# Kernel optimization log

Hardware: AMD Instinct MI355X
Metric: run time of the kernel (lower is better)

The kernel has to match this reference:

```python
import jax, jax.numpy as jnp
import numpy as np

N_NODES = 50000
N_EDGES = 400000
IN_DIM = 8
HIDDEN = 768
N_LAYERS = 4
LN_EPS = 1e-5


def setup_inputs() -> dict:
    key = jax.random.key(0)
    ks = jax.random.split(key, 10)
    x = jax.random.normal(ks[0], (N_NODES, IN_DIM), dtype=jnp.float32)
    edge_index = jax.random.randint(ks[1], (2, N_EDGES), 0, N_NODES, dtype=jnp.int32)
    # input projection
    s_in = 1.0 / np.sqrt(IN_DIM)
    Wp = jax.random.uniform(ks[2], (HIDDEN, IN_DIM), jnp.float32, -s_in, s_in)
    bp = jax.random.uniform(ks[3], (HIDDEN,), jnp.float32, -s_in, s_in)
    # stacked per-layer SAGEConv params (all layers have out_c == HIDDEN here)
    s_h = 1.0 / np.sqrt(HIDDEN)
    Wl = jax.random.uniform(ks[4], (N_LAYERS, HIDDEN, HIDDEN), jnp.float32, -s_h, s_h)  # lin_l (aggregated neighbors), has bias
    bl = jax.random.uniform(ks[5], (N_LAYERS, HIDDEN), jnp.float32, -s_h, s_h)
    Wr = jax.random.uniform(ks[6], (N_LAYERS, HIDDEN, HIDDEN), jnp.float32, -s_h, s_h)  # lin_r (root), no bias
    # LayerNorm params
    gamma = jnp.ones((N_LAYERS, HIDDEN), dtype=jnp.float32)
    beta = jnp.zeros((N_LAYERS, HIDDEN), dtype=jnp.float32)
    return {"x": x, "Wp": Wp, "bp": bp, "Wl": Wl, "bl": bl, "Wr": Wr,
            "gamma": gamma, "beta": beta, "edge_index": edge_index}


def _layer_norm(h, g, b):
    mu = jnp.mean(h, axis=-1, keepdims=True)
    var = jnp.mean(jnp.square(h - mu), axis=-1, keepdims=True)
    return (h - mu) * jax.lax.rsqrt(var + LN_EPS) * g + b


def reference(x, Wp, bp, Wl, bl, Wr, gamma, beta, edge_index):
    n = x.shape[0]
    src, dst = edge_index[0], edge_index[1]
    # in-degree per target node, clamped for mean
    deg = jax.ops.segment_sum(jnp.ones_like(dst, dtype=x.dtype), dst, num_segments=n)
    inv_deg = 1.0 / jnp.maximum(deg, 1.0)

    h = x @ Wp.T + bp  # [N, HIDDEN]

    def layer(h, params):
        Wl_i, bl_i, Wr_i, g_i, b_i = params
        # mean aggregation of source features at targets: [N, C]
        agg = jax.ops.segment_sum(h[src], dst, num_segments=n) * inv_deg[:, None]
        out = agg @ Wl_i.T + bl_i + h @ Wr_i.T  # SAGEConv
        out = _layer_norm(jax.nn.silu(out), g_i, b_i)  # norm(silu(conv))
        return out, None

    h, _ = jax.lax.scan(layer, h, (Wl, bl, Wr, gamma, beta))
    return h
```

## Files before the change

kernel.cpp:

```cpp
#include <hip/hip_runtime.h>

#define NN 50000
#define NE 400000
#define HID 768
#define NL 4

typedef short bf16x8_t __attribute__((ext_vector_type(8)));
typedef float f32x4_t __attribute__((ext_vector_type(4)));

__device__ __forceinline__ unsigned short f2bf(float f) {
  union { float f; unsigned int u; } c; c.f = f;
  unsigned int u = c.u;
  u += 0x7FFF + ((u >> 16) & 1);
  return (unsigned short)(u >> 16);
}
__device__ __forceinline__ float bf2f(unsigned short s) {
  union { unsigned int u; float f; } c; c.u = ((unsigned int)s) << 16;
  return c.f;
}

__device__ __forceinline__ void async16(const void* g, void* l) {
  __builtin_amdgcn_global_load_lds((const __attribute__((address_space(1))) void*)g,
                                   (__attribute__((address_space(3))) void*)l,
                                   16, 0, 0);
}

__global__ void k_zero2(int* __restrict__ a, int* __restrict__ b, int n) {
  int i = blockIdx.x * blockDim.x + threadIdx.x;
  if (i < n) { a[i] = 0; b[i] = 0; }
}

__global__ void k_cvt(const float* __restrict__ a, unsigned short* __restrict__ o, int n) {
  int i = blockIdx.x * blockDim.x + threadIdx.x;
  if (i < n) o[i] = f2bf(a[i]);
}

__global__ __launch_bounds__(256) void k_inproj(const float* __restrict__ x,
                                                const float* __restrict__ Wp,
                                                const float* __restrict__ bp,
                                                unsigned short* __restrict__ h) {
  int n = blockIdx.x;
  __shared__ float xs[8];
  if (threadIdx.x < 8) xs[threadIdx.x] = x[n * 8 + threadIdx.x];
  __syncthreads();
  for (int j = threadIdx.x; j < HID; j += 256) {
    const float* w = Wp + j * 8;
    float s = bp[j];
#pragma unroll
    for (int k = 0; k < 8; ++k) s += xs[k] * w[k];
    h[(size_t)n * HID + j] = f2bf(s);
  }
}

__global__ void k_deg(const int* __restrict__ dst, int* __restrict__ deg) {
  int i = blockIdx.x * blockDim.x + threadIdx.x;
  if (i < NE) atomicAdd(&deg[dst[i]], 1);
}

__global__ __launch_bounds__(1024) void k_scan(const int* __restrict__ deg, int* __restrict__ rowptr) {
  __shared__ int sm[1024];
  const int chunk = 49;
  int t = threadIdx.x;
  int start = t * chunk;
  int end = min(start + chunk, NN);
  int local = 0;
  for (int i = start; i < end; ++i) local += deg[i];
  sm[t] = local;
  __syncthreads();
  for (int off = 1; off < 1024; off <<= 1) {
    int v = (t >= off) ? sm[t - off] : 0;
    __syncthreads();
    sm[t] += v;
    __syncthreads();
  }
  int run = sm[t] - local;
  for (int i = start; i < end; ++i) { rowptr[i] = run; run += deg[i]; }
  if (start < NN && end == NN) rowptr[NN] = run;
}

__global__ void k_fill(const int* __restrict__ src, const int* __restrict__ dst,
                       const int* __restrict__ rowptr, int* __restrict__ cursor,
                       int* __restrict__ csr) {
  int i = blockIdx.x * blockDim.x + threadIdx.x;
  if (i < NE) {
    int d = dst[i];
    int pos = atomicAdd(&cursor[d], 1);
    csr[rowptr[d] + pos] = src[i];
  }
}

__global__ __launch_bounds__(192) void k_agg(const unsigned short* __restrict__ h,
                                             const int* __restrict__ csr,
                                             const int* __restrict__ rowptr,
                                             unsigned short* __restrict__ agg) {
  int n = blockIdx.x;
  int t = threadIdx.x;
  int beg = rowptr[n], end = rowptr[n + 1];
  float a0 = 0.f, a1 = 0.f, a2 = 0.f, a3 = 0.f;
  for (int i = beg; i < end; ++i) {
    int s = csr[i];
    ushort4 v = *(const ushort4*)(h + (size_t)s * HID + t * 4);
    a0 += bf2f(v.x); a1 += bf2f(v.y); a2 += bf2f(v.z); a3 += bf2f(v.w);
  }
  float inv = 1.0f / (float)max(end - beg, 1);
  ushort4 o;
  o.x = f2bf(a0 * inv); o.y = f2bf(a1 * inv); o.z = f2bf(a2 * inv); o.w = f2bf(a3 * inv);
  *(ushort4*)(agg + (size_t)n * HID + t * 4) = o;
}

#define BM 128
#define BN 128
#define BK 32
#define NBAND 391

__global__ __launch_bounds__(256) void k_gemm(const unsigned short* __restrict__ A0,
                                              const unsigned short* __restrict__ A1,
                                              const unsigned short* __restrict__ B0,
                                              const unsigned short* __restrict__ B1,
                                              const float* __restrict__ bias,
                                              unsigned short* __restrict__ sact, int M) {
  int b = blockIdx.x;
  int xcd = b & 7;
  int rest = b >> 3;
  int nt6 = rest % 6;
  int g = rest / 6;
  int mband = g * 8 + xcd;
  if (mband >= NBAND) return;
  int m0 = mband * BM;
  int n0 = nt6 * BN;

  __shared__ unsigned short As[BM * BK];
  __shared__ unsigned short Bs[BN * BK];
  f32x4_t acc[4][4] = {};
  int tid = threadIdx.x;
  int lane = tid & 63, w = tid >> 6;
  int wr = w >> 1, wc = w & 1;
  int r4 = lane >> 2;
  int cg = (lane & 3) ^ ((lane >> 3) & 3);
  int cs = cg * 8;

  for (int phase = 0; phase < 2; ++phase) {
    const unsigned short* A = phase ? A1 : A0;
    const unsigned short* B = phase ? B1 : B0;
    for (int k0 = 0; k0 < HID; k0 += BK) {
      __syncthreads();
#pragma unroll
      for (int c = 0; c < 2; ++c) {
        int seg = w * 32 + c * 16;
        int row = seg + r4;
        async16(A + (size_t)(m0 + row) * HID + k0 + cs, &As[seg * BK]);
        async16(B + (size_t)(n0 + row) * HID + k0 + cs, &Bs[seg * BK]);
      }
      __syncthreads();
      bf16x8_t af[4], bfr[4];
      int q = lane >> 4;
      int mr = lane & 15;
      int sq = (q ^ ((mr >> 1) & 3)) * 8;
#pragma unroll
      for (int t = 0; t < 4; ++t) {
        af[t]  = *(const bf16x8_t*)(&As[(wr * 64 + t * 16 + mr) * BK + sq]);
        bfr[t] = *(const bf16x8_t*)(&Bs[(wc * 64 + t * 16 + mr) * BK + sq]);
      }
#pragma unroll
      for (int mt = 0; mt < 4; ++mt)
#pragma unroll
        for (int nt = 0; nt < 4; ++nt)
          acc[mt][nt] = __builtin_amdgcn_mfma_f32_16x16x32_bf16(af[mt], bfr[nt], acc[mt][nt], 0, 0, 0);
    }
  }
  int col = lane & 15;
  int rq = (lane >> 4) * 4;
#pragma unroll
  for (int mt = 0; mt < 4; ++mt) {
#pragma unroll
    for (int nt = 0; nt < 4; ++nt) {
      int j = n0 + wc * 64 + nt * 16 + col;
      float bv = bias[j];
#pragma unroll
      for (int r = 0; r < 4; ++r) {
        int gm = m0 + wr * 64 + mt * 16 + rq + r;
        if (gm < M) {
          float v = acc[mt][nt][r] + bv;
          float s = v / (1.f + __expf(-v));
          sact[(size_t)gm * HID + j] = f2bf(s);
        }
      }
    }
  }
}

__global__ __launch_bounds__(256) void k_ln(const unsigned short* __restrict__ sact,
                                            const float* __restrict__ gamma,
                                            const float* __restrict__ beta,
                                            unsigned short* __restrict__ hout,
                                            float* __restrict__ fout) {
  int n = blockIdx.x;
  const unsigned short* p = sact + (size_t)n * HID;
  float v[3];
  float sum = 0.f, sq = 0.f;
#pragma unroll
  for (int i = 0; i < 3; ++i) {
    float s = bf2f(p[threadIdx.x + i * 256]);
    v[i] = s; sum += s; sq += s * s;
  }
#pragma unroll
  for (int off = 32; off >= 1; off >>= 1) {
    sum += __shfl_down(sum, off);
    sq  += __shfl_down(sq, off);
  }
  __shared__ float rs[4], rq2[4];
  int wv = threadIdx.x >> 6;
  if ((threadIdx.x & 63) == 0) { rs[wv] = sum; rq2[wv] = sq; }
  __syncthreads();
  if (threadIdx.x == 0) {
    float s = rs[0] + rs[1] + rs[2] + rs[3];
    float q = rq2[0] + rq2[1] + rq2[2] + rq2[3];
    rs[0] = s / (float)HID;
    rq2[0] = q / (float)HID;
  }
  __syncthreads();
  float mu = rs[0];
  float var = rq2[0] - mu * mu;
  float inv = rsqrtf(var + 1e-5f);
#pragma unroll
  for (int i = 0; i < 3; ++i) {
    int j = threadIdx.x + i * 256;
    float y = (v[i] - mu) * inv * gamma[j] + beta[j];
    if (fout) fout[(size_t)n * HID + j] = y;
    else      hout[(size_t)n * HID + j] = f2bf(y);
  }
}

extern "C" void kernel_launch(void* const* d_in, const int* in_sizes, int n_in,
                              void* d_out, int out_size, void* d_ws, size_t ws_size,
                              hipStream_t stream) {
  const float* x     = (const float*)d_in[0];
  const float* Wp    = (const float*)d_in[1];
  const float* bp    = (const float*)d_in[2];
  const float* Wl    = (const float*)d_in[3];
  const float* bl    = (const float*)d_in[4];
  const float* Wr    = (const float*)d_in[5];
  const float* gamma = (const float*)d_in[6];
  const float* beta  = (const float*)d_in[7];
  const int*   ei    = (const int*)d_in[8];
  float* out = (float*)d_out;

  const int* src = ei;
  const int* dst = ei + NE;

  char* p = (char*)d_ws;
  unsigned short* h    = (unsigned short*)p;              p += (size_t)NN * HID * 2;
  unsigned short* agg  = (unsigned short*)p;              p += (size_t)NN * HID * 2;
  unsigned short* sact = (unsigned short*)p;              p += (size_t)NN * HID * 2;
  unsigned short* Wlb  = (unsigned short*)p;              p += (size_t)NL * HID * HID * 2;
  unsigned short* Wrb  = (unsigned short*)p;              p += (size_t)NL * HID * HID * 2;
  int* deg             = (int*)p;                         p += (size_t)NN * 4;
  int* rowptr          = (int*)p;                         p += (size_t)(NN + 1) * 4 + 12;
  int* cursor          = (int*)p;                         p += (size_t)NN * 4;
  int* csr             = (int*)p;                         p += (size_t)NE * 4;

  k_zero2<<<(NN + 255) / 256, 256, 0, stream>>>(deg, cursor, NN);
  int wn = NL * HID * HID;
  k_cvt<<<(wn + 255) / 256, 256, 0, stream>>>(Wl, Wlb, wn);
  k_cvt<<<(wn + 255) / 256, 256, 0, stream>>>(Wr, Wrb, wn);
  k_inproj<<<NN, 256, 0, stream>>>(x, Wp, bp, h);
  k_deg<<<(NE + 255) / 256, 256, 0, stream>>>(dst, deg);
  k_scan<<<1, 1024, 0, stream>>>(deg, rowptr);
  k_fill<<<(NE + 255) / 256, 256, 0, stream>>>(src, dst, rowptr, cursor, csr);

  int ggrid = 8 * 6 * ((NBAND + 7) / 8);
  for (int l = 0; l < NL; ++l) {
    k_agg<<<NN, 192, 0, stream>>>(h, csr, rowptr, agg);
    k_gemm<<<ggrid, 256, 0, stream>>>(agg, h,
                                      Wlb + (size_t)l * HID * HID,
                                      Wrb + (size_t)l * HID * HID,
                                      bl + (size_t)l * HID, sact, NN);
    k_ln<<<NN, 256, 0, stream>>>(sact, gamma + (size_t)l * HID, beta + (size_t)l * HID,
                                 h, (l == NL - 1) ? out : nullptr);
  }
}
```

Measured before the change: 1.701 ms.

## Enlarge GEMM tiles to 224x256 and double-buffer async LDS loads

Replaces the 128x128 GEMM tile with a 224x256 tile computed by 512 threads. The two K phases (aggregated and root inputs) are fused into one 48-step loop. Global-to-LDS async loads are double-buffered, with explicit vmcnt waits and MFMA priority raised, so loads for step T+2 overlap compute on step T. The intent is more operand reuse per tile and better latency hiding, at the cost of higher register and LDS pressure. Each stage loads 256 A rows even though only 224 are used, so the last band reads past the end of the input rows.

```diff
diff --git a/kernel.cpp b/kernel.cpp
--- a/kernel.cpp
+++ b/kernel.cpp
@@ -108,77 +108,107 @@
   *(ushort4*)(agg + (size_t)n * HID + t * 4) = o;
 }
 
-#define BM 128
-#define BN 128
-#define BK 32
-#define NBAND 391
-
-__global__ __launch_bounds__(256) void k_gemm(const unsigned short* __restrict__ A0,
-                                              const unsigned short* __restrict__ A1,
-                                              const unsigned short* __restrict__ B0,
-                                              const unsigned short* __restrict__ B1,
-                                              const float* __restrict__ bias,
-                                              unsigned short* __restrict__ sact, int M) {
+#define BM 224
+#define BN 256
+#define BKT 32
+#define NKT 48
+#define NBANDS 224
+
+__global__ __launch_bounds__(512, 2) void k_gemm(const unsigned short* __restrict__ A0,
+                                                 const unsigned short* __restrict__ A1,
+                                                 const unsigned short* __restrict__ B0,
+                                                 const unsigned short* __restrict__ B1,
+                                                 const float* __restrict__ bias,
+                                                 unsigned short* __restrict__ sact, int M) {
+  __shared__ __align__(16) unsigned short As[2][256 * BKT];
+  __shared__ __align__(16) unsigned short Bs[2][256 * BKT];
+
   int b = blockIdx.x;
   int xcd = b & 7;
   int rest = b >> 3;
-  int nt6 = rest % 6;
-  int g = rest / 6;
+  int nt3 = rest % 3;
+  int g = rest / 3;
   int mband = g * 8 + xcd;
-  if (mband >= NBAND) return;
   int m0 = mband * BM;
-  int n0 = nt6 * BN;
-
-  __shared__ unsigned short As[BM * BK];
-  __shared__ unsigned short Bs[BN * BK];
-  f32x4_t acc[4][4] = {};
+  int n0 = nt3 * BN;
+
   int tid = threadIdx.x;
-  int lane = tid & 63, w = tid >> 6;
-  int wr = w >> 1, wc = w & 1;
-  int r4 = lane >> 2;
-  int cg = (lane & 3) ^ ((lane >> 3) & 3);
-  int cs = cg * 8;
-
-  for (int phase = 0; phase < 2; ++phase) {
-    const unsigned short* A = phase ? A1 : A0;
-    const unsigned short* B = phase ? B1 : B0;
-    for (int k0 = 0; k0 < HID; k0 += BK) {
-      __syncthreads();
-#pragma unroll
-      for (int c = 0; c < 2; ++c) {
-        int seg = w * 32 + c * 16;
-        int row = seg + r4;
-        async16(A + (size_t)(m0 + row) * HID + k0 + cs, &As[seg * BK]);
-        async16(B + (size_t)(n0 + row) * HID + k0 + cs, &Bs[seg * BK]);
-      }
-      __syncthreads();
-      bf16x8_t af[4], bfr[4];
-      int q = lane >> 4;
-      int mr = lane & 15;
-      int sq = (q ^ ((mr >> 1) & 3)) * 8;
-#pragma unroll
-      for (int t = 0; t < 4; ++t) {
-        af[t]  = *(const bf16x8_t*)(&As[(wr * 64 + t * 16 + mr) * BK + sq]);
-        bfr[t] = *(const bf16x8_t*)(&Bs[(wc * 64 + t * 16 + mr) * BK + sq]);
-      }
-#pragma unroll
-      for (int mt = 0; mt < 4; ++mt)
-#pragma unroll
-        for (int nt = 0; nt < 4; ++nt)
-          acc[mt][nt] = __builtin_amdgcn_mfma_f32_16x16x32_bf16(af[mt], bfr[nt], acc[mt][nt], 0, 0, 0);
-    }
-  }
+  int lane = tid & 63;
+  int w = tid >> 6;
+  int wm = w >> 2, wn = w & 3;
+
+  int srow = w * 16 + (lane >> 2);
+  int kgg = (lane & 3) ^ ((srow >> 1) & 3);
+  size_t aoffg = (size_t)(m0 + srow) * HID + kgg * 8;
+  size_t boffg = (size_t)(n0 + srow) * HID + kgg * 8;
+  const size_t rstep = (size_t)128 * HID;
+
+  auto stage = [&](int kt, int slot) {
+    const unsigned short* A = (kt < 24) ? A0 : A1;
+    const unsigned short* B = (kt < 24) ? B0 : B1;
+    size_t kk = (size_t)((kt < 24) ? kt : kt - 24) * BKT;
+    async16(A + aoffg + kk,         &As[slot][(w * 16) * BKT]);
+    async16(B + boffg + kk,         &Bs[slot][(w * 16) * BKT]);
+    async16(A + aoffg + rstep + kk, &As[slot][(128 + w * 16) * BKT]);
+    async16(B + boffg + rstep + kk, &Bs[slot][(128 + w * 16) * BKT]);
+  };
+
+  int mr = lane & 15, kq = lane >> 4;
+  int aoff[7], boff[4];
+#pragma unroll
+  for (int t = 0; t < 7; ++t) {
+    int row = wm * 112 + t * 16 + mr;
+    aoff[t] = row * BKT + ((kq ^ ((row >> 1) & 3)) * 8);
+  }
+#pragma unroll
+  for (int t = 0; t < 4; ++t) {
+    int row = wn * 64 + t * 16 + mr;
+    boff[t] = row * BKT + ((kq ^ ((row >> 1) & 3)) * 8);
+  }
+
+  f32x4_t acc[7][4] = {};
+
+  stage(0, 0);
+  stage(1, 1);
+
+#pragma unroll 2
+  for (int T = 0; T < NKT; ++T) {
+    int slot = T & 1;
+    if (T < NKT - 1) asm volatile("s_waitcnt vmcnt(4)" ::: "memory");
+    else             asm volatile("s_waitcnt vmcnt(0)" ::: "memory");
+    __builtin_amdgcn_s_barrier();
+    asm volatile("" ::: "memory");
+
+    bf16x8_t af[7], bf[4];
+#pragma unroll
+    for (int t = 0; t < 7; ++t) af[t] = *(const bf16x8_t*)&As[slot][aoff[t]];
+#pragma unroll
+    for (int t = 0; t < 4; ++t) bf[t] = *(const bf16x8_t*)&Bs[slot][boff[t]];
+
+    __builtin_amdgcn_s_setprio(1);
+#pragma unroll
+    for (int mt = 0; mt < 7; ++mt)
+#pragma unroll
+      for (int nt = 0; nt < 4; ++nt)
+        acc[mt][nt] = __builtin_amdgcn_mfma_f32_16x16x32_bf16(af[mt], bf[nt], acc[mt][nt], 0, 0, 0);
+    __builtin_amdgcn_s_setprio(0);
+
+    asm volatile("s_waitcnt lgkmcnt(0)" ::: "memory");
+    __builtin_amdgcn_s_barrier();
+    if (T + 2 < NKT) stage(T + 2, slot);
+  }
+
   int col = lane & 15;
   int rq = (lane >> 4) * 4;
 #pragma unroll
-  for (int mt = 0; mt < 4; ++mt) {
+  for (int mt = 0; mt < 7; ++mt) {
 #pragma unroll
     for (int nt = 0; nt < 4; ++nt) {
-      int j = n0 + wc * 64 + nt * 16 + col;
+      int j = n0 + wn * 64 + nt * 16 + col;
       float bv = bias[j];
 #pragma unroll
       for (int r = 0; r < 4; ++r) {
-        int gm = m0 + wr * 64 + mt * 16 + rq + r;
+        int gm = m0 + wm * 112 + mt * 16 + rq + r;
         if (gm < M) {
           float v = acc[mt][nt][r] + bv;
           float s = v / (1.f + __expf(-v));
@@ -268,10 +298,10 @@
   k_scan<<<1, 1024, 0, stream>>>(deg, rowptr);
   k_fill<<<(NE + 255) / 256, 256, 0, stream>>>(src, dst, rowptr, cursor, csr);
 
-  int ggrid = 8 * 6 * ((NBAND + 7) / 8);
+  const int ggrid = 8 * 3 * 28;
   for (int l = 0; l < NL; ++l) {
     k_agg<<<NN, 192, 0, stream>>>(h, csr, rowptr, agg);
-    k_gemm<<<ggrid, 256, 0, stream>>>(agg, h,
+    k_gemm<<<ggrid, 512, 0, stream>>>(agg, h,
                                       Wlb + (size_t)l * HID * HID,
                                       Wrb + (size_t)l * HID * HID,
                                       bl + (size_t)l * HID, sact, NN);
```

Result: no change. 1.673 ms (-1.7%).
